# Kernel optimization log

Hardware: AMD Instinct MI355X
Metric: run time of the kernel (lower is better)

## Reference

```python
import jax, jax.numpy as jnp
import numpy as np
import math

B, L, D = 4, 2048, 1024        # batch, x_len, x_dim
QKV, H = 64, 16                # qkv_dim, head_dim (number of heads)


def setup_inputs() -> dict:
    key = jax.random.key(0)
    ks = jax.random.split(key, 10)
    s = 1.0 / math.sqrt(D)
    return {
        "x": jax.random.normal(ks[0], (B, L, D), jnp.float32),
        "encoder_x": jax.random.normal(ks[1], (B, L, D), jnp.float32),
        "Wq": jax.random.normal(ks[2], (D, QKV * H), jnp.float32) * s,
        "bq": jax.random.normal(ks[3], (QKV * H,), jnp.float32) * 0.01,
        "Wk": jax.random.normal(ks[4], (D, QKV * H), jnp.float32) * s,
        "bk": jax.random.normal(ks[5], (QKV * H,), jnp.float32) * 0.01,
        "Wv": jax.random.normal(ks[6], (D, QKV * H), jnp.float32) * s,
        "bv": jax.random.normal(ks[7], (QKV * H,), jnp.float32) * 0.01,
        "Wo": jax.random.normal(ks[8], (QKV * H, D), jnp.float32) * s,
        "bo": jax.random.normal(ks[9], (D,), jnp.float32) * 0.01,
    }


def reference(x, encoder_x, Wq, bq, Wk, bk, Wv, bv, Wo, bo):
    # q,k from encoder_x; v from x  -> [B, L, H, QKV]
    q = (encoder_x @ Wq + bq).reshape(B, L, H, QKV)
    k = (encoder_x @ Wk + bk).reshape(B, L, H, QKV)
    v = (x @ Wv + bv).reshape(B, L, H, QKV)
    # explicit [B,H,L,L] score matrix + softmax over k (faithful to source)
    scores = jax.nn.softmax(
        jnp.einsum("bqhd,bkhd->bhqk", q, k) / math.sqrt(QKV), axis=-1
    )
    # faithful to source einsum 'bvhd,bhqk->bvhd': no shared contraction
    # index, so scores are summed over (q,k) and broadcast onto v per (b,h).
    attn = jnp.einsum("bvhd,bhqk->bvhd", v, scores).reshape(B, L, H * QKV)
    return attn @ Wo + bo
```

## Files before the change

### kernel.cpp

```cpp
#include <hip/hip_runtime.h>
#include <stdint.h>


typedef __attribute__((ext_vector_type(8))) short bf16x8;
typedef __attribute__((ext_vector_type(4))) float f32x4;

typedef __attribute__((address_space(1))) void as1_void;
typedef __attribute__((address_space(3))) void as3_void;
#define GLD16(g, s)                                                          \
  __builtin_amdgcn_global_load_lds((as1_void*)(g), (as3_void*)(s), 16, 0, 0)

__device__ __forceinline__ short f2bf(float f) {
  union { float f; uint32_t u; } v; v.f = f;
  uint32_t r = v.u + 0x7FFFu + ((v.u >> 16) & 1u);
  return (short)(r >> 16);
}

__device__ __forceinline__ bf16x8 pack8(f32x4 a, f32x4 b) {
  union { f32x4 f; uint32_t u[4]; } x, y;
  x.f = a; y.f = b;
#pragma unroll
  for (int t = 0; t < 4; ++t) x.u[t] += 0x8000u;
#pragma unroll
  for (int t = 0; t < 4; ++t) y.u[t] += 0x8000u;
  union { bf16x8 v; uint32_t u[4]; } o;
  o.u[0] = __builtin_amdgcn_perm(x.u[1], x.u[0], 0x07060302);
  o.u[1] = __builtin_amdgcn_perm(x.u[3], x.u[2], 0x07060302);
  o.u[2] = __builtin_amdgcn_perm(y.u[1], y.u[0], 0x07060302);
  o.u[3] = __builtin_amdgcn_perm(y.u[3], y.u[2], 0x07060302);
  return o.v;
}

__global__ __launch_bounds__(256) void prep_w(
    const float* __restrict__ Wo, short* __restrict__ wot,
    const float* __restrict__ bv, const float* __restrict__ bo,
    float* __restrict__ biasc) {
  constexpr int N = 1024, D = 1024;
  __shared__ union {
    float tile[64][65];
    float red[256];
  } sm;
  const int b = blockIdx.x, tid = threadIdx.x;

  if (b < 256) {
    const int br = (b >> 4) * 64, bc = (b & 15) * 64;
#pragma unroll
    for (int t = 0; t < 16; ++t) {
      int idx = t * 256 + tid;
      int r = idx >> 6, c = idx & 63;
      sm.tile[r][c] = Wo[(size_t)(br + r) * N + bc + c];
    }
    __syncthreads();
#pragma unroll
    for (int t = 0; t < 16; ++t) {
      int idx = t * 256 + tid;
      int r = idx >> 6, c = idx & 63;
      wot[(size_t)(bc + r) * N + br + c] = f2bf(sm.tile[c][r]);
    }
  } else {
    const int b3 = b - 256;
    const int nx = tid & 15, ky = tid >> 4;
    const int n = b3 * 16 + nx;
    float s = 0.f;
    for (int k = ky; k < D; k += 16)
      s += bv[k] * Wo[(size_t)k * N + n];
    sm.red[tid] = s;
    __syncthreads();
#pragma unroll
    for (int st = 128; st >= 16; st >>= 1) {
      if (tid < st) sm.red[tid] += sm.red[tid + st];
      __syncthreads();
    }
    if (ky == 0) biasc[n] = 2048.0f * sm.red[nx] + bo[n];
  }
}

__global__ __launch_bounds__(256) void mid(
    const float* __restrict__ x, short* __restrict__ x_bf,
    const short* __restrict__ Wot, const float* __restrict__ Wv,
    short* __restrict__ Wt) {
  constexpr int BK = 64, N = 1024, K = 1024;
  __shared__ __align__(16) short As[32 * BK];
  __shared__ __align__(16) float Bsf[64 * BK];
  const int b = blockIdx.x, tid = threadIdx.x;

  if (b >= 512) {
    const int i = (b - 512) * 256 + tid;
    const float4* p = (const float4*)x;
    float4 a = p[2 * (size_t)i], c = p[2 * (size_t)i + 1];
    bf16x8 o;
    o[0] = f2bf(a.x); o[1] = f2bf(a.y); o[2] = f2bf(a.z); o[3] = f2bf(a.w);
    o[4] = f2bf(c.x); o[5] = f2bf(c.y); o[6] = f2bf(c.z); o[7] = f2bf(c.w);
    *(bf16x8*)(x_bf + 8 * (size_t)i) = o;
    return;
  }

  const int lane = tid & 63, wave = tid >> 6;
  const int bm = (b >> 4) * 32, bn = (b & 15) * 64;
  const int wm = (wave & 1) * 16, wn = (wave >> 1) * 32;
  const int l15 = lane & 15, quad = lane >> 4;

  f32x4 acc[2];
  acc[0] = (f32x4){0.f, 0.f, 0.f, 0.f};
  acc[1] = (f32x4){0.f, 0.f, 0.f, 0.f};

  const int ar = tid >> 3, ac8 = (tid & 7) ^ (ar & 7);
  const short* pa = Wot + (size_t)(bm + ar) * K + ac8 * 8;
  short* la = As + tid * 8;
  const int br = tid >> 4, bc4 = (tid & 15) ^ (br & 7);
  const float* pb = Wv + (size_t)(bn + br) * K + bc4 * 4;
  float* lb = Bsf + tid * 4;

  for (int kt = 0; kt < K; kt += BK) {
    GLD16(pa, la);
#pragma unroll
    for (int s = 0; s < 4; ++s) GLD16(pb + (size_t)(16 * s) * K, lb + 1024 * s);
    pa += BK; pb += BK;
    __syncthreads();
#pragma unroll
    for (int kk = 0; kk < 2; ++kk) {
      const int r = wm + l15;
      bf16x8 af =
          *(const bf16x8*)(As + r * BK + ((kk * 4 + quad) ^ (r & 7)) * 8);
#pragma unroll
      for (int j = 0; j < 2; ++j) {
        const int rn = wn + j * 16 + l15;
        const int c4 = kk * 8 + quad * 2;
        f32x4 u0 = *(const f32x4*)(Bsf + (rn * 16 + (c4 ^ (rn & 7))) * 4);
        f32x4 u1 = *(const f32x4*)(Bsf + (rn * 16 + ((c4 + 1) ^ (rn & 7))) * 4);
        acc[j] = __builtin_amdgcn_mfma_f32_16x16x32_bf16(af, pack8(u0, u1),
                                                         acc[j], 0, 0, 0);
      }
    }
    __syncthreads();
  }
#pragma unroll
  for (int j = 0; j < 2; ++j) {
    const int col = bn + wn + j * 16 + l15;
    const int row0 = bm + wm + quad * 4;
#pragma unroll
    for (int r = 0; r < 4; ++r)
      Wt[(size_t)(row0 + r) * N + col] = f2bf(2048.f * acc[j][r]);
  }
}

__global__ __launch_bounds__(256) void gemm_main(
    const short* __restrict__ A, const short* __restrict__ Bt,
    const float* __restrict__ bias, float* __restrict__ Out,
    int M, int N, int K) {
  constexpr int BK = 64;
  __shared__ __align__(16) char smem[32768];
  short* As = (short*)smem;
  short* Bs = (short*)(smem + 16384);
  const int tid = threadIdx.x, lane = tid & 63, wave = tid >> 6;
  const int b = blockIdx.x;
  const int bm = (b & 63) * 128;
  const int bn = (b >> 6) * 128;
  const int wm = (wave & 1) * 64, wn = (wave >> 1) * 64;
  const int l15 = lane & 15, quad = lane >> 4;

  f32x4 acc[4][4];
#pragma unroll
  for (int i = 0; i < 4; ++i)
#pragma unroll
    for (int j = 0; j < 4; ++j) acc[i][j] = (f32x4){0.f, 0.f, 0.f, 0.f};

  const int srow = tid >> 3, sc8 = (tid & 7) ^ (srow & 7);
  const short* pa = A + (size_t)(bm + srow) * K + sc8 * 8;
  const short* pb = Bt + (size_t)(bn + srow) * K + sc8 * 8;
  short* la = As + tid * 8;
  short* lb = Bs + tid * 8;

  for (int kt = 0; kt < K; kt += BK) {
#pragma unroll
    for (int s = 0; s < 4; ++s) GLD16(pa + (size_t)(32 * s) * K, la + 2048 * s);
#pragma unroll
    for (int s = 0; s < 4; ++s) GLD16(pb + (size_t)(32 * s) * K, lb + 2048 * s);
    pa += BK; pb += BK;
    __syncthreads();
#pragma unroll
    for (int kk = 0; kk < 2; ++kk) {
      bf16x8 af[4], bfr[4];
#pragma unroll
      for (int i = 0; i < 4; ++i) {
        const int r = wm + i * 16 + l15;
        af[i] = *(const bf16x8*)(As + r * BK + ((kk * 4 + quad) ^ (r & 7)) * 8);
      }
#pragma unroll
      for (int j = 0; j < 4; ++j) {
        const int r = wn + j * 16 + l15;
        bfr[j] = *(const bf16x8*)(Bs + r * BK + ((kk * 4 + quad) ^ (r & 7)) * 8);
      }
#pragma unroll
      for (int i = 0; i < 4; ++i)
#pragma unroll
        for (int j = 0; j < 4; ++j)
          acc[i][j] = __builtin_amdgcn_mfma_f32_16x16x32_bf16(
              af[i], bfr[j], acc[i][j], 0, 0, 0);
    }
    __syncthreads();
  }

  float* T = (float*)smem + wave * 1088;
#pragma unroll
  for (int i = 0; i < 4; ++i) {
#pragma unroll
    for (int j = 0; j < 4; ++j) {
      const float bb = bias[bn + wn + j * 16 + l15];
#pragma unroll
      for (int r = 0; r < 4; ++r)
        T[(quad * 4 + r) * 68 + j * 16 + l15] = acc[i][j][r] + bb;
    }
#pragma unroll
    for (int p = 0; p < 4; ++p) {
      const int row = (lane >> 4) + 4 * p;
      const int ch = lane & 15;
      f32x4 v = *(const f32x4*)(T + row * 68 + ch * 4);
      *(f32x4*)(Out + (size_t)(bm + wm + i * 16 + row) * N + bn + wn +
                ch * 4) = v;
    }
  }
}

extern "C" void kernel_launch(void* const* d_in, const int* in_sizes, int n_in,
                              void* d_out, int out_size, void* d_ws,
                              size_t ws_size, hipStream_t stream) {
  const float* x  = (const float*)d_in[0];
  const float* Wv = (const float*)d_in[6];
  const float* bv = (const float*)d_in[7];
  const float* Wo = (const float*)d_in[8];
  const float* bo = (const float*)d_in[9];
  float* out = (float*)d_out;

  constexpr int L = 2048, D = 1024, NO = 1024;
  constexpr int M = 4 * L;

  char* ws = (char*)d_ws;
  short* x_bf   = (short*)(ws);
  short* wot_bf = (short*)(ws + (16u << 20));
  short* wt_bf  = (short*)(ws + (18u << 20));
  float* biasc  = (float*)(ws + (20u << 20));

  prep_w<<<320, 256, 0, stream>>>(Wo, wot_bf, bv, bo, biasc);
  mid<<<4608, 256, 0, stream>>>(x, x_bf, wot_bf, Wv, wt_bf);
  gemm_main<<<(M / 128) * (NO / 128), 256, 0, stream>>>(
      x_bf, wt_bf, biasc, out, M, NO, D);
}
```

Baseline: 177.3 us.

## Fuse x bf16 conversion into main GEMM and Wo transpose into weight GEMM

Removes the separate pass that converts x to bf16: the main GEMM now loads fp32 x with regular loads, packs it to bf16 in registers and writes it into the swizzled LDS tile. The Wo transpose/convert step is also folded into the weight-product kernel, which reads Wo directly through a padded LDS tile, cutting the work to two kernel launches. This saves a 32 MB write and re-read of x_bf plus one launch. In exchange the main GEMM reads twice as many bytes for A and loses async global_load_lds for that operand, which may reduce overlap and add register pressure.

Measured after the change: 165.3 us. 1.07x faster.

```diff
diff --git a/kernel.cpp b/kernel.cpp
--- a/kernel.cpp
+++ b/kernel.cpp
@@ -31,67 +31,31 @@
   return o.v;
 }
 
-__global__ __launch_bounds__(256) void prep_w(
-    const float* __restrict__ Wo, short* __restrict__ wot,
+__global__ __launch_bounds__(256) void wgemm(
+    const float* __restrict__ Wo, const float* __restrict__ Wv,
     const float* __restrict__ bv, const float* __restrict__ bo,
-    float* __restrict__ biasc) {
-  constexpr int N = 1024, D = 1024;
-  __shared__ union {
-    float tile[64][65];
-    float red[256];
-  } sm;
+    short* __restrict__ Wt, float* __restrict__ biasc) {
+  constexpr int BK = 64, NW = 1024;
+  __shared__ __align__(16) float Bsf[64 * BK];
+  __shared__ __align__(16) float Ts[64 * 36];
   const int b = blockIdx.x, tid = threadIdx.x;
 
-  if (b < 256) {
-    const int br = (b >> 4) * 64, bc = (b & 15) * 64;
-#pragma unroll
-    for (int t = 0; t < 16; ++t) {
-      int idx = t * 256 + tid;
-      int r = idx >> 6, c = idx & 63;
-      sm.tile[r][c] = Wo[(size_t)(br + r) * N + bc + c];
-    }
-    __syncthreads();
-#pragma unroll
-    for (int t = 0; t < 16; ++t) {
-      int idx = t * 256 + tid;
-      int r = idx >> 6, c = idx & 63;
-      wot[(size_t)(bc + r) * N + br + c] = f2bf(sm.tile[c][r]);
-    }
-  } else {
-    const int b3 = b - 256;
+  if (b >= 512) {
+    float* red = Bsf;
+    const int b3 = b - 512;
     const int nx = tid & 15, ky = tid >> 4;
     const int n = b3 * 16 + nx;
     float s = 0.f;
-    for (int k = ky; k < D; k += 16)
-      s += bv[k] * Wo[(size_t)k * N + n];
-    sm.red[tid] = s;
+    for (int k = ky; k < 1024; k += 16)
+      s += bv[k] * Wo[(size_t)k * NW + n];
+    red[tid] = s;
     __syncthreads();
 #pragma unroll
     for (int st = 128; st >= 16; st >>= 1) {
-      if (tid < st) sm.red[tid] += sm.red[tid + st];
+      if (tid < st) red[tid] += red[tid + st];
       __syncthreads();
     }
-    if (ky == 0) biasc[n] = 2048.0f * sm.red[nx] + bo[n];
-  }
-}
-
-__global__ __launch_bounds__(256) void mid(
-    const float* __restrict__ x, short* __restrict__ x_bf,
-    const short* __restrict__ Wot, const float* __restrict__ Wv,
-    short* __restrict__ Wt) {
-  constexpr int BK = 64, N = 1024, K = 1024;
-  __shared__ __align__(16) short As[32 * BK];
-  __shared__ __align__(16) float Bsf[64 * BK];
-  const int b = blockIdx.x, tid = threadIdx.x;
-
-  if (b >= 512) {
-    const int i = (b - 512) * 256 + tid;
-    const float4* p = (const float4*)x;
-    float4 a = p[2 * (size_t)i], c = p[2 * (size_t)i + 1];
-    bf16x8 o;
-    o[0] = f2bf(a.x); o[1] = f2bf(a.y); o[2] = f2bf(a.z); o[3] = f2bf(a.w);
-    o[4] = f2bf(c.x); o[5] = f2bf(c.y); o[6] = f2bf(c.z); o[7] = f2bf(c.w);
-    *(bf16x8*)(x_bf + 8 * (size_t)i) = o;
+    if (ky == 0) biasc[n] = 2048.0f * red[nx] + bo[n];
     return;
   }
 
@@ -104,24 +68,31 @@
   acc[0] = (f32x4){0.f, 0.f, 0.f, 0.f};
   acc[1] = (f32x4){0.f, 0.f, 0.f, 0.f};
 
-  const int ar = tid >> 3, ac8 = (tid & 7) ^ (ar & 7);
-  const short* pa = Wot + (size_t)(bm + ar) * K + ac8 * 8;
-  short* la = As + tid * 8;
   const int br = tid >> 4, bc4 = (tid & 15) ^ (br & 7);
-  const float* pb = Wv + (size_t)(bn + br) * K + bc4 * 4;
+  const float* pb = Wv + (size_t)(bn + br) * NW + bc4 * 4;
   float* lb = Bsf + tid * 4;
 
-  for (int kt = 0; kt < K; kt += BK) {
-    GLD16(pa, la);
-#pragma unroll
-    for (int s = 0; s < 4; ++s) GLD16(pb + (size_t)(16 * s) * K, lb + 1024 * s);
-    pa += BK; pb += BK;
+  const int ajr = tid >> 3, ac4 = (tid & 7) * 4;
+  const float* pa = Wo + (size_t)ajr * NW + bm + ac4;
+
+  for (int kt = 0; kt < 1024; kt += BK) {
+    float4 va = *(const float4*)(pa);
+    float4 vb = *(const float4*)(pa + 32 * (size_t)NW);
+    pa += (size_t)BK * NW;
+#pragma unroll
+    for (int s = 0; s < 4; ++s) GLD16(pb + (size_t)(16 * s) * NW, lb + 1024 * s);
+    pb += BK;
+    *(float4*)(Ts + ajr * 36 + ac4) = va;
+    *(float4*)(Ts + (ajr + 32) * 36 + ac4) = vb;
     __syncthreads();
 #pragma unroll
     for (int kk = 0; kk < 2; ++kk) {
-      const int r = wm + l15;
-      bf16x8 af =
-          *(const bf16x8*)(As + r * BK + ((kk * 4 + quad) ^ (r & 7)) * 8);
+      const float* tsp = Ts + ((kk * 4 + quad) * 8) * 36 + wm + l15;
+      float av[8];
+#pragma unroll
+      for (int e = 0; e < 8; ++e) av[e] = tsp[e * 36];
+      bf16x8 af = pack8((f32x4){av[0], av[1], av[2], av[3]},
+                        (f32x4){av[4], av[5], av[6], av[7]});
 #pragma unroll
       for (int j = 0; j < 2; ++j) {
         const int rn = wn + j * 16 + l15;
@@ -140,12 +111,12 @@
     const int row0 = bm + wm + quad * 4;
 #pragma unroll
     for (int r = 0; r < 4; ++r)
-      Wt[(size_t)(row0 + r) * N + col] = f2bf(2048.f * acc[j][r]);
+      Wt[(size_t)(row0 + r) * NW + col] = f2bf(2048.f * acc[j][r]);
   }
 }
 
 __global__ __launch_bounds__(256) void gemm_main(
-    const short* __restrict__ A, const short* __restrict__ Bt,
+    const float* __restrict__ X, const short* __restrict__ Bt,
     const float* __restrict__ bias, float* __restrict__ Out,
     int M, int N, int K) {
   constexpr int BK = 64;
@@ -166,17 +137,28 @@
     for (int j = 0; j < 4; ++j) acc[i][j] = (f32x4){0.f, 0.f, 0.f, 0.f};
 
   const int srow = tid >> 3, sc8 = (tid & 7) ^ (srow & 7);
-  const short* pa = A + (size_t)(bm + srow) * K + sc8 * 8;
+  const float* pa = X + (size_t)(bm + srow) * K + sc8 * 8;
   const short* pb = Bt + (size_t)(bn + srow) * K + sc8 * 8;
   short* la = As + tid * 8;
   short* lb = Bs + tid * 8;
 
   for (int kt = 0; kt < K; kt += BK) {
-#pragma unroll
-    for (int s = 0; s < 4; ++s) GLD16(pa + (size_t)(32 * s) * K, la + 2048 * s);
+    float4 a0[4], a1[4];
+#pragma unroll
+    for (int s = 0; s < 4; ++s) {
+      const float* p = pa + (size_t)(32 * s) * K;
+      a0[s] = *(const float4*)(p);
+      a1[s] = *(const float4*)(p + 4);
+    }
 #pragma unroll
     for (int s = 0; s < 4; ++s) GLD16(pb + (size_t)(32 * s) * K, lb + 2048 * s);
     pa += BK; pb += BK;
+#pragma unroll
+    for (int s = 0; s < 4; ++s) {
+      *(bf16x8*)(la + 2048 * s) =
+          pack8((f32x4){a0[s].x, a0[s].y, a0[s].z, a0[s].w},
+                (f32x4){a1[s].x, a1[s].y, a1[s].z, a1[s].w});
+    }
     __syncthreads();
 #pragma unroll
     for (int kk = 0; kk < 2; ++kk) {
@@ -232,17 +214,14 @@
   const float* bo = (const float*)d_in[9];
   float* out = (float*)d_out;
 
-  constexpr int L = 2048, D = 1024, NO = 1024;
-  constexpr int M = 4 * L;
+  constexpr int D = 1024, NO = 1024;
+  constexpr int M = 8192;
 
   char* ws = (char*)d_ws;
-  short* x_bf   = (short*)(ws);
-  short* wot_bf = (short*)(ws + (16u << 20));
-  short* wt_bf  = (short*)(ws + (18u << 20));
-  float* biasc  = (float*)(ws + (20u << 20));
-
-  prep_w<<<320, 256, 0, stream>>>(Wo, wot_bf, bv, bo, biasc);
-  mid<<<4608, 256, 0, stream>>>(x, x_bf, wot_bf, Wv, wt_bf);
+  short* wt_bf = (short*)(ws);
+  float* biasc = (float*)(ws + (2u << 20));
+
+  wgemm<<<576, 256, 0, stream>>>(Wo, Wv, bv, bo, wt_bf, biasc);
   gemm_main<<<(M / 128) * (NO / 128), 256, 0, stream>>>(
-      x_bf, wt_bf, biasc, out, M, NO, D);
-}
+      x, wt_bf, biasc, out, M, NO, D);
+}
```
